# Kernel optimization log

Measured on AMD Instinct MI355X. Metric: run time of the kernel, lower is better.

The kernel has to match this reference:

```python
import jax, jax.numpy as jnp
import numpy as np

B, A, S, T, H = 512, 100, 7, 11, 1024  # batch, n_agents, n_car_states, n_frame_history, hidden
IN = S * T  # 77 = input_size of embedding Linear


def setup_inputs() -> dict:
    key = jax.random.key(0)
    ks = jax.random.split(key, 8)
    scale = 1.0 / np.sqrt(H)
    return {
        "inputs": jax.random.normal(ks[0], (B, A * S, T), dtype=jnp.float32),
        "h0": jnp.zeros((1, B, H), dtype=jnp.float32),
        "c0": jnp.zeros((1, B, H), dtype=jnp.float32),
        "W_emb": jax.random.normal(ks[1], (H, IN), dtype=jnp.float32) * (1.0 / np.sqrt(IN)),
        "b_emb": jax.random.normal(ks[2], (H,), dtype=jnp.float32) * (1.0 / np.sqrt(IN)),
        "W_ih": jax.random.normal(ks[3], (4 * H, H), dtype=jnp.float32) * scale,
        "W_hh": jax.random.normal(ks[4], (4 * H, H), dtype=jnp.float32) * scale,
        "b_ih": jax.random.normal(ks[5], (4 * H,), dtype=jnp.float32) * scale,
        "b_hh": jax.random.normal(ks[6], (4 * H,), dtype=jnp.float32) * scale,
    }


def reference(inputs, h0, c0, W_emb, b_emb, W_ih, W_hh, b_ih, b_hh):
    # Batched embedding of all agents at once (replaces the per-agent Python loop):
    # inputs [B, A*S, T] -> [B, A, S*T] -> embed -> [A, B, H]
    x = inputs.reshape(B, A, S, T).reshape(B, A, IN)
    embedded = jnp.einsum('bai,hi->abh', x, W_emb) + b_emb  # [A, B, H]

    bias = b_ih + b_hh  # fuse the two LSTM biases

    def step(carry, x_t):
        h, c = carry  # each [B, H]
        gates = x_t @ W_ih.T + h @ W_hh.T + bias  # [B, 4H]
        i, f, g, o = jnp.split(gates, 4, axis=-1)  # PyTorch gate order i,f,g,o
        c = jax.nn.sigmoid(f) * c + jax.nn.sigmoid(i) * jnp.tanh(g)
        h = jax.nn.sigmoid(o) * jnp.tanh(c)
        return (h, c), h

    (h_f, c_f), output = jax.lax.scan(step, (h0[0], c0[0]), embedded)
    return output, h_f[None], c_f[None]  # output [A, B, H], (h, c) [1, B, H]
```

## Files before the change

kernel.cpp:

```cpp
#include <hip/hip_runtime.h>

typedef _Float16 f16;
typedef __attribute__((ext_vector_type(8))) _Float16 f16x8;
typedef __attribute__((ext_vector_type(4))) _Float16 f16x4;
typedef __attribute__((ext_vector_type(4))) float floatx4;

#define BB 512
#define AA 100
#define HH 1024
#define KX 96
#define KTOT 1120
#define NKC (KTOT / 32)
#define WSTR 1120
#define ASTR 1128


__global__ __launch_bounds__(256) void cast_whh_k(const float* __restrict__ whh,
                                                  f16* __restrict__ wcat) {
  int gid = blockIdx.x * 256 + threadIdx.x;
  int n = gid >> 8, k4 = (gid & 255) << 2;
  float4 v = *(const float4*)(whh + (size_t)n * HH + k4);
  f16x4 o; o[0] = (f16)v.x; o[1] = (f16)v.y; o[2] = (f16)v.z; o[3] = (f16)v.w;
  *(f16x4*)(wcat + (size_t)n * WSTR + k4) = o;
}

__global__ __launch_bounds__(512) void prep_wcomb_k(
    const float* __restrict__ wih, const float* __restrict__ wemb,
    const float* __restrict__ bemb, const float* __restrict__ bih,
    const float* __restrict__ bhh, f16* __restrict__ wcat,
    float* __restrict__ bcomb) {
  __shared__ float part[4][128];
  int n = blockIdx.x;
  int q = threadIdx.x >> 7, j = threadIdx.x & 127;
  float acc = 0.f;
  const float* wrow = wih + (size_t)n * HH + q * 256;
  if (j < 77) {
    const float* we = wemb + (size_t)(q * 256) * 77 + j;
    #pragma unroll 4
    for (int m = 0; m < 256; ++m) acc += wrow[m] * we[(size_t)m * 77];
  } else if (j == 96) {
    const float* be = bemb + q * 256;
    #pragma unroll 4
    for (int m = 0; m < 256; ++m) acc += wrow[m] * be[m];
  }
  part[q][j] = acc;
  __syncthreads();
  if (q == 0 && j < 97) {
    float s = part[0][j] + part[1][j] + part[2][j] + part[3][j];
    if (j < 96) {
      wcat[(size_t)n * WSTR + 1024 + j] = (f16)s;
    } else {
      bcomb[n] = s + bih[n] + bhh[n];
    }
  }
}

__global__ __launch_bounds__(256) void cast_x_k(const float* __restrict__ in,
                                                f16* __restrict__ xh) {
  int gid = blockIdx.x * 256 + threadIdx.x;
  int row = gid / 96;
  int i = gid - row * 96;
  int t = row >> 9, b = row & 511;
  f16 v = (f16)0.f;
  if (i < 77) v = (f16)in[(size_t)b * 7700 + t * 77 + i];
  xh[(size_t)row * KX + i] = v;
}

__global__ __launch_bounds__(256) void init_hc_k(const float* __restrict__ h0,
                                                 const float* __restrict__ c0,
                                                 f16* __restrict__ h16,
                                                 float* __restrict__ cws) {
  int gid = blockIdx.x * 256 + threadIdx.x;
  h16[gid] = (f16)h0[gid];
  cws[gid] = c0[gid];
}


__device__ __forceinline__ float sigm(float x) { return 1.f / (1.f + __expf(-x)); }

__global__ __launch_bounds__(256) void lstm_step_k(
    const f16* __restrict__ wcat, const float* __restrict__ bcomb,
    const f16* __restrict__ xh, const f16* __restrict__ hin,
    f16* __restrict__ hout, float* __restrict__ cws,
    float* __restrict__ outh, int t) {
  __shared__ __align__(16) char smem[32 * ASTR * 2];
  f16* alds = (f16*)smem;
  float (*glds)[32][34] = (float (*)[32][34])smem;

  int tid = threadIdx.x;
  int id = blockIdx.x;
  int xcd = id & 7, slot = id >> 3;
  int hb = xcd * 4 + (slot >> 4);
  int mb = slot & 15;
  int m0 = mb * 32, h0 = hb * 32;

  for (int v = tid; v < 32 * 140; v += 256) {
    int row = v / 140, c8 = v - row * 140;
    int bg = m0 + row;
    const f16* src = (c8 < 128)
        ? (hin + (size_t)bg * HH + c8 * 8)
        : (xh + ((size_t)(t * BB + bg)) * KX + (c8 - 128) * 8);
    *(f16x8*)(alds + row * ASTR + c8 * 8) = *(const f16x8*)src;
  }
  __syncthreads();

  int w = tid >> 6, lane = tid & 63;
  int lr = lane & 15, lk = lane >> 4;

  int aoff0 = lr * ASTR + lk * 8;
  int aoff1 = (16 + lr) * ASTR + lk * 8;

  const f16* bp0 = wcat + (size_t)(w * HH + h0 + lr) * WSTR + lk * 8;
  const f16* bp1 = wcat + (size_t)(w * HH + h0 + 16 + lr) * WSTR + lk * 8;

  floatx4 acc00 = {0.f, 0.f, 0.f, 0.f};
  floatx4 acc01 = acc00, acc10 = acc00, acc11 = acc00;

  #pragma unroll 5
  for (int kc = 0; kc < NKC; ++kc) {
    f16x8 a0 = *(const f16x8*)(alds + aoff0 + kc * 32);
    f16x8 a1 = *(const f16x8*)(alds + aoff1 + kc * 32);
    f16x8 b0 = *(const f16x8*)(bp0 + kc * 32);
    f16x8 b1 = *(const f16x8*)(bp1 + kc * 32);
    acc00 = __builtin_amdgcn_mfma_f32_16x16x32_f16(a0, b0, acc00, 0, 0, 0);
    acc10 = __builtin_amdgcn_mfma_f32_16x16x32_f16(a1, b0, acc10, 0, 0, 0);
    acc01 = __builtin_amdgcn_mfma_f32_16x16x32_f16(a0, b1, acc01, 0, 0, 0);
    acc11 = __builtin_amdgcn_mfma_f32_16x16x32_f16(a1, b1, acc11, 0, 0, 0);
  }

  __syncthreads();
  #pragma unroll
  for (int r = 0; r < 4; ++r) {
    glds[w][lk * 4 + r][lr]           = acc00[r];
    glds[w][lk * 4 + r][16 + lr]      = acc01[r];
    glds[w][16 + lk * 4 + r][lr]      = acc10[r];
    glds[w][16 + lk * 4 + r][16 + lr] = acc11[r];
  }
  __syncthreads();

  #pragma unroll
  for (int e = tid; e < 32 * 32; e += 256) {
    int row = e >> 5, col = e & 31;
    int bg = m0 + row, hc = h0 + col;
    float gi = glds[0][row][col] + bcomb[hc];
    float gf = glds[1][row][col] + bcomb[HH + hc];
    float gg = glds[2][row][col] + bcomb[2 * HH + hc];
    float go = glds[3][row][col] + bcomb[3 * HH + hc];
    float iv = sigm(gi), fv = sigm(gf), gv = tanhf(gg), ov = sigm(go);
    size_t idx = (size_t)bg * HH + hc;
    float cn = fv * cws[idx] + iv * gv;
    float hn = ov * tanhf(cn);
    cws[idx] = cn;
    outh[idx] = hn;
    hout[idx] = (f16)hn;
  }
}


extern "C" void kernel_launch(void* const* d_in, const int* in_sizes, int n_in,
                              void* d_out, int out_size, void* d_ws, size_t ws_size,
                              hipStream_t stream) {
  const float* inputs = (const float*)d_in[0];
  const float* h0     = (const float*)d_in[1];
  const float* c0     = (const float*)d_in[2];
  const float* W_emb  = (const float*)d_in[3];
  const float* b_emb  = (const float*)d_in[4];
  const float* W_ih   = (const float*)d_in[5];
  const float* W_hh   = (const float*)d_in[6];
  const float* b_ih   = (const float*)d_in[7];
  const float* b_hh   = (const float*)d_in[8];
  float* out = (float*)d_out;

  char* ws = (char*)d_ws;
  f16*   Wcat  = (f16*)(ws);
  f16*   xh    = (f16*)(ws + 9175040);
  f16*   h16a  = (f16*)(ws + 19005440);
  f16*   h16b  = (f16*)(ws + 20054016);
  float* c_ws  = (float*)(ws + 21102592);
  float* bcomb = (float*)(ws + 23199744);

  cast_whh_k  <<<4096, 256, 0, stream>>>(W_hh, Wcat);
  prep_wcomb_k<<<4096, 512, 0, stream>>>(W_ih, W_emb, b_emb, b_ih, b_hh, Wcat, bcomb);
  cast_x_k    <<<19200, 256, 0, stream>>>(inputs, xh);
  init_hc_k   <<<2048, 256, 0, stream>>>(h0, c0, h16a, c_ws);

  for (int t = 0; t < 100; ++t) {
    const f16* hin = (t & 1) ? h16b : h16a;
    f16* hout      = (t & 1) ? h16a : h16b;
    lstm_step_k<<<512, 256, 0, stream>>>(Wcat, bcomb, xh, hin, hout, c_ws,
                                         out + (size_t)t * BB * HH, t);
  }

  hipMemcpyAsync(out + (size_t)AA * BB * HH,
                 out + (size_t)99 * BB * HH,
                 (size_t)BB * HH * sizeof(float), hipMemcpyDeviceToDevice, stream);
  hipMemcpyAsync(out + (size_t)AA * BB * HH + (size_t)BB * HH,
                 c_ws,
                 (size_t)BB * HH * sizeof(float), hipMemcpyDeviceToDevice, stream);
}
```

Baseline: 2.483 ms.

## Shrink LSTM step tiles, read A directly from global, MFMA-ize weight prep

The per-step LSTM kernel now uses 32x16 output tiles with 1024 blocks instead of 32x32 with 512 blocks. It reads h and x fragments straight from global memory rather than staging the full 32x1120 A tile in LDS, which cuts LDS use and the sync before the MFMA loop. The fused W_ih·W_emb precompute is rewritten as an MFMA GEMM over a transposed fp16 W_emb, with the embedding bias folded in as an extra column. The costs are that each h row is fetched by twice as many blocks, A loads become strided global loads, and the bias path now goes through fp16 rounding of W_ih.

```diff
diff --git a/kernel.cpp b/kernel.cpp
--- a/kernel.cpp
+++ b/kernel.cpp
@@ -10,9 +10,7 @@
 #define HH 1024
 #define KX 96
 #define KTOT 1120
-#define NKC (KTOT / 32)
 #define WSTR 1120
-#define ASTR 1128
 
 
 __global__ __launch_bounds__(256) void cast_whh_k(const float* __restrict__ whh,
@@ -24,35 +22,53 @@
   *(f16x4*)(wcat + (size_t)n * WSTR + k4) = o;
 }
 
-__global__ __launch_bounds__(512) void prep_wcomb_k(
-    const float* __restrict__ wih, const float* __restrict__ wemb,
-    const float* __restrict__ bemb, const float* __restrict__ bih,
-    const float* __restrict__ bhh, f16* __restrict__ wcat,
-    float* __restrict__ bcomb) {
-  __shared__ float part[4][128];
-  int n = blockIdx.x;
-  int q = threadIdx.x >> 7, j = threadIdx.x & 127;
-  float acc = 0.f;
-  const float* wrow = wih + (size_t)n * HH + q * 256;
-  if (j < 77) {
-    const float* we = wemb + (size_t)(q * 256) * 77 + j;
-    #pragma unroll 4
-    for (int m = 0; m < 256; ++m) acc += wrow[m] * we[(size_t)m * 77];
-  } else if (j == 96) {
-    const float* be = bemb + q * 256;
-    #pragma unroll 4
-    for (int m = 0; m < 256; ++m) acc += wrow[m] * be[m];
-  }
-  part[q][j] = acc;
+__global__ __launch_bounds__(256) void cast_wembT_k(const float* __restrict__ wemb,
+                                                    const float* __restrict__ bemb,
+                                                    f16* __restrict__ wembT) {
+  int gid = blockIdx.x * 256 + threadIdx.x;
+  int i = gid >> 10, k = gid & 1023;
+  float v = 0.f;
+  if (i < 77) v = wemb[(size_t)k * 77 + i];
+  else if (i == 77) v = bemb[k];
+  wembT[gid] = (f16)v;
+}
+
+__global__ __launch_bounds__(256) void prep_gemm_k(
+    const float* __restrict__ wih, const f16* __restrict__ wembT,
+    const float* __restrict__ bih, const float* __restrict__ bhh,
+    f16* __restrict__ wcat, float* __restrict__ bcomb) {
+  __shared__ __align__(16) f16 alds[64][1032];
+  int tid = threadIdx.x;
+  int n0 = blockIdx.x * 64;
+  for (int v = tid; v < 64 * 256; v += 256) {
+    int row = v >> 8, c4 = (v & 255) << 2;
+    float4 s = *(const float4*)(wih + (size_t)(n0 + row) * HH + c4);
+    f16x4 o; o[0] = (f16)s.x; o[1] = (f16)s.y; o[2] = (f16)s.z; o[3] = (f16)s.w;
+    *(f16x4*)(&alds[row][c4]) = o;
+  }
   __syncthreads();
-  if (q == 0 && j < 97) {
-    float s = part[0][j] + part[1][j] + part[2][j] + part[3][j];
-    if (j < 96) {
-      wcat[(size_t)n * WSTR + 1024 + j] = (f16)s;
-    } else {
-      bcomb[n] = s + bih[n] + bhh[n];
+  int w = tid >> 6, lane = tid & 63, lr = lane & 15, lk = lane >> 4;
+  floatx4 acc[6];
+  #pragma unroll
+  for (int j = 0; j < 6; ++j) acc[j] = (floatx4){0.f, 0.f, 0.f, 0.f};
+  for (int kc = 0; kc < 32; ++kc) {
+    f16x8 a = *(const f16x8*)(&alds[w * 16 + lr][kc * 32 + lk * 8]);
+    #pragma unroll
+    for (int j = 0; j < 6; ++j) {
+      f16x8 b = *(const f16x8*)(wembT + (size_t)(j * 16 + lr) * 1024 + kc * 32 + lk * 8);
+      acc[j] = __builtin_amdgcn_mfma_f32_16x16x32_f16(a, b, acc[j], 0, 0, 0);
     }
   }
+  #pragma unroll
+  for (int j = 0; j < 6; ++j)
+    #pragma unroll
+    for (int r = 0; r < 4; ++r) {
+      int n = n0 + w * 16 + lk * 4 + r;
+      int i = j * 16 + lr;
+      float v = acc[j][r];
+      if (i == 77) bcomb[n] = v + bih[n] + bhh[n];
+      wcat[(size_t)n * WSTR + 1024 + i] = (i == 77) ? (f16)0.f : (f16)v;
+    }
 }
 
 __global__ __launch_bounds__(256) void cast_x_k(const float* __restrict__ in,
@@ -78,69 +94,57 @@
 
 __device__ __forceinline__ float sigm(float x) { return 1.f / (1.f + __expf(-x)); }
 
-__global__ __launch_bounds__(256) void lstm_step_k(
+__global__ __launch_bounds__(256, 4) void lstm_step_k(
     const f16* __restrict__ wcat, const float* __restrict__ bcomb,
     const f16* __restrict__ xh, const f16* __restrict__ hin,
     f16* __restrict__ hout, float* __restrict__ cws,
     float* __restrict__ outh, int t) {
-  __shared__ __align__(16) char smem[32 * ASTR * 2];
-  f16* alds = (f16*)smem;
-  float (*glds)[32][34] = (float (*)[32][34])smem;
-
+  __shared__ float glds[4][32][18];
   int tid = threadIdx.x;
   int id = blockIdx.x;
   int xcd = id & 7, slot = id >> 3;
-  int hb = xcd * 4 + (slot >> 4);
+  int hb = xcd * 8 + (slot >> 4);
   int mb = slot & 15;
-  int m0 = mb * 32, h0 = hb * 32;
-
-  for (int v = tid; v < 32 * 140; v += 256) {
-    int row = v / 140, c8 = v - row * 140;
-    int bg = m0 + row;
-    const f16* src = (c8 < 128)
-        ? (hin + (size_t)bg * HH + c8 * 8)
-        : (xh + ((size_t)(t * BB + bg)) * KX + (c8 - 128) * 8);
-    *(f16x8*)(alds + row * ASTR + c8 * 8) = *(const f16x8*)src;
+  int m0 = mb * 32, h0 = hb * 16;
+
+  int w = tid >> 6, lane = tid & 63, lr = lane & 15, lk = lane >> 4;
+
+  const f16* ap0 = hin + (size_t)(m0 + lr) * HH + lk * 8;
+  const f16* ap1 = ap0 + 16 * HH;
+  const f16* bp  = wcat + (size_t)(w * HH + h0 + lr) * WSTR + lk * 8;
+
+  floatx4 acc0 = {0.f, 0.f, 0.f, 0.f};
+  floatx4 acc1 = acc0;
+
+  #pragma unroll 8
+  for (int kc = 0; kc < 32; ++kc) {
+    f16x8 a0 = *(const f16x8*)(ap0 + kc * 32);
+    f16x8 a1 = *(const f16x8*)(ap1 + kc * 32);
+    f16x8 b  = *(const f16x8*)(bp + kc * 32);
+    acc0 = __builtin_amdgcn_mfma_f32_16x16x32_f16(a0, b, acc0, 0, 0, 0);
+    acc1 = __builtin_amdgcn_mfma_f32_16x16x32_f16(a1, b, acc1, 0, 0, 0);
+  }
+  const f16* xp0 = xh + ((size_t)(t * BB) + m0 + lr) * KX + lk * 8;
+  const f16* xp1 = xp0 + 16 * KX;
+  #pragma unroll
+  for (int kc = 0; kc < 3; ++kc) {
+    f16x8 a0 = *(const f16x8*)(xp0 + kc * 32);
+    f16x8 a1 = *(const f16x8*)(xp1 + kc * 32);
+    f16x8 b  = *(const f16x8*)(bp + (32 + kc) * 32);
+    acc0 = __builtin_amdgcn_mfma_f32_16x16x32_f16(a0, b, acc0, 0, 0, 0);
+    acc1 = __builtin_amdgcn_mfma_f32_16x16x32_f16(a1, b, acc1, 0, 0, 0);
+  }
+
+  #pragma unroll
+  for (int r = 0; r < 4; ++r) {
+    glds[w][lk * 4 + r][lr]      = acc0[r];
+    glds[w][16 + lk * 4 + r][lr] = acc1[r];
   }
   __syncthreads();
 
-  int w = tid >> 6, lane = tid & 63;
-  int lr = lane & 15, lk = lane >> 4;
-
-  int aoff0 = lr * ASTR + lk * 8;
-  int aoff1 = (16 + lr) * ASTR + lk * 8;
-
-  const f16* bp0 = wcat + (size_t)(w * HH + h0 + lr) * WSTR + lk * 8;
-  const f16* bp1 = wcat + (size_t)(w * HH + h0 + 16 + lr) * WSTR + lk * 8;
-
-  floatx4 acc00 = {0.f, 0.f, 0.f, 0.f};
-  floatx4 acc01 = acc00, acc10 = acc00, acc11 = acc00;
-
-  #pragma unroll 5
-  for (int kc = 0; kc < NKC; ++kc) {
-    f16x8 a0 = *(const f16x8*)(alds + aoff0 + kc * 32);
-    f16x8 a1 = *(const f16x8*)(alds + aoff1 + kc * 32);
-    f16x8 b0 = *(const f16x8*)(bp0 + kc * 32);
-    f16x8 b1 = *(const f16x8*)(bp1 + kc * 32);
-    acc00 = __builtin_amdgcn_mfma_f32_16x16x32_f16(a0, b0, acc00, 0, 0, 0);
-    acc10 = __builtin_amdgcn_mfma_f32_16x16x32_f16(a1, b0, acc10, 0, 0, 0);
-    acc01 = __builtin_amdgcn_mfma_f32_16x16x32_f16(a0, b1, acc01, 0, 0, 0);
-    acc11 = __builtin_amdgcn_mfma_f32_16x16x32_f16(a1, b1, acc11, 0, 0, 0);
-  }
-
-  __syncthreads();
-  #pragma unroll
-  for (int r = 0; r < 4; ++r) {
-    glds[w][lk * 4 + r][lr]           = acc00[r];
-    glds[w][lk * 4 + r][16 + lr]      = acc01[r];
-    glds[w][16 + lk * 4 + r][lr]      = acc10[r];
-    glds[w][16 + lk * 4 + r][16 + lr] = acc11[r];
-  }
-  __syncthreads();
-
-  #pragma unroll
-  for (int e = tid; e < 32 * 32; e += 256) {
-    int row = e >> 5, col = e & 31;
+  #pragma unroll
+  for (int e = tid; e < 32 * 16; e += 256) {
+    int row = e >> 4, col = e & 15;
     int bg = m0 + row, hc = h0 + col;
     float gi = glds[0][row][col] + bcomb[hc];
     float gf = glds[1][row][col] + bcomb[HH + hc];
@@ -178,17 +182,19 @@
   f16*   h16b  = (f16*)(ws + 20054016);
   float* c_ws  = (float*)(ws + 21102592);
   float* bcomb = (float*)(ws + 23199744);
+  f16*   wembT = (f16*)(ws + 23216128);
 
   cast_whh_k  <<<4096, 256, 0, stream>>>(W_hh, Wcat);
-  prep_wcomb_k<<<4096, 512, 0, stream>>>(W_ih, W_emb, b_emb, b_ih, b_hh, Wcat, bcomb);
+  cast_wembT_k<<<384, 256, 0, stream>>>(W_emb, b_emb, wembT);
+  prep_gemm_k <<<64, 256, 0, stream>>>(W_ih, wembT, b_ih, b_hh, Wcat, bcomb);
   cast_x_k    <<<19200, 256, 0, stream>>>(inputs, xh);
   init_hc_k   <<<2048, 256, 0, stream>>>(h0, c0, h16a, c_ws);
 
   for (int t = 0; t < 100; ++t) {
     const f16* hin = (t & 1) ? h16b : h16a;
     f16* hout      = (t & 1) ? h16a : h16b;
-    lstm_step_k<<<512, 256, 0, stream>>>(Wcat, bcomb, xh, hin, hout, c_ws,
-                                         out + (size_t)t * BB * HH, t);
+    lstm_step_k<<<1024, 256, 0, stream>>>(Wcat, bcomb, xh, hin, hout, c_ws,
+                                          out + (size_t)t * BB * HH, t);
   }
 
   hipMemcpyAsync(out + (size_t)AA * BB * HH,
```

After: 4.377 ms. +76.3%, slower.
